# Optimization experiments

Hardware: AMD Instinct MI355X
Metric: run time of the kernel (lower is better)

The kernel has to match this reference:

```python
import jax, jax.numpy as jnp
import numpy as np

EPS_LN = 1e-5
EPS_BN = 1e-5

B, S, N, F, H, E, L = 8, 16, 1024, 16, 128, 32768, 4


def _layernorm(h, g, b):
    mu = h.mean(-1, keepdims=True)
    var = ((h - mu) ** 2).mean(-1, keepdims=True)
    return (h - mu) / jnp.sqrt(var + EPS_LN) * g + b


def setup_inputs() -> dict:
    key = jax.random.key(0)
    ks = iter(jax.random.split(key, 40))
    nrm = lambda shape, s=0.05: jax.random.normal(next(ks), shape, dtype=jnp.float32) * s
    inp = {
        'x': jax.random.normal(next(ks), (B, S, N, F), dtype=jnp.float32),
        'edge_index': jax.random.randint(next(ks), (2, E), 0, N, dtype=jnp.int32),
        'edge_weights': jax.random.uniform(next(ks), (E,), dtype=jnp.float32),
        'edge_features': jax.random.normal(next(ks), (E, 1), dtype=jnp.float32),
        # input projection: Linear(F,H) + LayerNorm(H)
        'w_in': nrm((F, H), 1.0 / np.sqrt(F)), 'b_in': nrm((H,)),
        'ln_in_g': jnp.ones((H,), jnp.float32), 'ln_in_b': jnp.zeros((H,), jnp.float32),
        # edge feature proj: Linear(1,H) -> ReLU -> Linear(H,1) -> Sigmoid
        'w_e1': nrm((1, H), 1.0), 'b_e1': nrm((H,)),
        'w_e2': nrm((H, 1), 1.0 / np.sqrt(H)), 'b_e2': nrm((1,)),
        # L GCN layers (weight [H,H], bias [H]) + BatchNorm1d affine params
        'gcn_w': nrm((L, H, H), 1.0 / np.sqrt(H)), 'gcn_b': nrm((L, H)),
        'bn_g': jnp.ones((L, H), jnp.float32), 'bn_b': jnp.zeros((L, H), jnp.float32),
        # 2-layer LSTM (PyTorch gate order i,f,g,o)
        'lstm_wih': nrm((2, 4 * H, H), 1.0 / np.sqrt(H)), 'lstm_whh': nrm((2, 4 * H, H), 1.0 / np.sqrt(H)),
        'lstm_bih': nrm((2, 4 * H)), 'lstm_bhh': nrm((2, 4 * H)),
        # output projection: Linear(H,H//2) + LayerNorm + Linear(H//2,1)
        'w_o1': nrm((H, H // 2), 1.0 / np.sqrt(H)), 'b_o1': nrm((H // 2,)),
        'ln_o_g': jnp.ones((H // 2,), jnp.float32), 'ln_o_b': jnp.zeros((H // 2,), jnp.float32),
        'w_o2': nrm((H // 2, 1), 1.0 / np.sqrt(H // 2)), 'b_o2': nrm((1,)),
    }
    return inp


def _forward(x, edge_index, edge_weights, edge_features,
             w_in, b_in, ln_in_g, ln_in_b, w_e1, b_e1, w_e2, b_e2,
             gcn_w, gcn_b, bn_g, bn_b,
             lstm_wih, lstm_whh, lstm_bih, lstm_bhh,
             w_o1, b_o1, ln_o_g, ln_o_b, w_o2, b_o2):
    Bs, Ss, Ns, Fs = x.shape
    BN = Bs * Ns
    # edge attention gating of edge weights
    e = jax.nn.relu(edge_features @ w_e1 + b_e1)
    att = jax.nn.sigmoid(e @ w_e2 + b_e2)[:, 0]            # [E]
    ew = edge_weights * att
    # input projection (dropout = identity in eval)
    h0 = jax.nn.relu(_layernorm(x @ w_in + b_in, ln_in_g, ln_in_b))   # [B,S,N,H]
    xf = h0.reshape(Bs * Ss, Ns, H)
    # replicate original slicing x[t:t+B] on the flattened (B*S) axis
    idx = jnp.arange(Ss)[:, None] + jnp.arange(Bs)[None, :]           # [S,B]
    hs = xf[idx].reshape(Ss, BN, H)                                   # [S,B*N,H]
    # GCN normalization (shared across timesteps): self-loops over all B*N nodes
    src = jnp.concatenate([edge_index[0], jnp.arange(BN, dtype=edge_index.dtype)])
    dst = jnp.concatenate([edge_index[1], jnp.arange(BN, dtype=edge_index.dtype)])
    w_sl = jnp.concatenate([ew, jnp.ones((BN,), ew.dtype)])
    deg = jax.ops.segment_sum(w_sl, dst, num_segments=BN)
    dis = jnp.where(deg > 0, jax.lax.rsqrt(jnp.where(deg > 0, deg, 1.0)), 0.0)
    norm = dis[src] * w_sl * dis[dst]                                  # [E+BN]
    # eval-mode BatchNorm (running mean 0, var 1)
    bn_scale = bn_g / np.sqrt(1.0 + EPS_BN)

    def gcn_block(h):                                                  # [BN,H]
        for l in range(L):
            identity = h
            hw = h @ gcn_w[l]
            m = jax.ops.segment_sum(hw[src] * norm[:, None], dst, num_segments=BN) + gcn_b[l]
            h = jax.nn.relu(m * bn_scale[l] + bn_b[l]) + identity
        return h

    hs = jax.vmap(gcn_block)(hs)                                       # [S,B*N,H]
    xt = jnp.transpose(hs.reshape(Ss, Bs, Ns, H), (1, 0, 2, 3))        # [B,S,N,H]
    # LSTM over the time axis for each (b,n) node sequence
    seq = jnp.transpose(xt, (0, 2, 1, 3)).reshape(BN, Ss, H)           # [B*N,S,H]

    def lstm_layer(seq, wih, whh, bih, bhh):
        def step(carry, xt):
            hprev, cprev = carry
            gates = xt @ wih.T + hprev @ whh.T + bih + bhh
            i, f, g, o = jnp.split(gates, 4, axis=-1)
            c = jax.nn.sigmoid(f) * cprev + jax.nn.sigmoid(i) * jnp.tanh(g)
            hn = jax.nn.sigmoid(o) * jnp.tanh(c)
            return (hn, c), hn
        z = jnp.zeros((seq.shape[0], H), seq.dtype)
        _, ys = jax.lax.scan(step, (z, z), jnp.swapaxes(seq, 0, 1))
        return jnp.swapaxes(ys, 0, 1)                                  # [B*N,S,H]

    y = lstm_layer(seq, lstm_wih[0], lstm_whh[0], lstm_bih[0], lstm_bhh[0])
    y = lstm_layer(y, lstm_wih[1], lstm_whh[1], lstm_bih[1], lstm_bhh[1])
    y = y[:, -1].reshape(Bs, Ns, H)
    z = jax.nn.relu(_layernorm(y @ w_o1 + b_o1, ln_o_g, ln_o_b))
    out = z @ w_o2 + b_o2                                              # [B,N,1]
    return out[..., None]                                              # [B,N,1,1]


def reference(x, edge_index, edge_weights, edge_features,
              w_in, b_in, ln_in_g, ln_in_b, w_e1, b_e1, w_e2, b_e2,
              gcn_w, gcn_b, bn_g, bn_b,
              lstm_wih, lstm_whh, lstm_bih, lstm_bhh,
              w_o1, b_o1, ln_o_g, ln_o_b, w_o2, b_o2):
    return _forward(x, edge_index, edge_weights, edge_features,
                    w_in, b_in, ln_in_g, ln_in_b, w_e1, b_e1, w_e2, b_e2,
                    gcn_w, gcn_b, bn_g, bn_b,
                    lstm_wih, lstm_whh, lstm_bih, lstm_bhh,
                    w_o1, b_o1, ln_o_g, ln_o_b, w_o2, b_o2)
```

## Files before the change

### kernel.cpp

```cpp
#include <hip/hip_runtime.h>
#include <cstdint>

#define EPS 1e-5f

typedef unsigned short ushort_t;
typedef __bf16 bf16x8 __attribute__((ext_vector_type(8)));
typedef float f32x4 __attribute__((ext_vector_type(4)));

__device__ __forceinline__ float sigm(float x) { return 1.f / (1.f + expf(-x)); }
__device__ __forceinline__ unsigned short f2bf(float f) {
    unsigned int u = __builtin_bit_cast(unsigned int, f);
    return (unsigned short)((u + 0x7fffu + ((u >> 16) & 1u)) >> 16);
}
__device__ __forceinline__ float bf2f(unsigned short s) {
    unsigned int u = ((unsigned int)s) << 16;
    return __builtin_bit_cast(float, u);
}
__device__ __forceinline__ float sigm_fast(float x) {
    float t = __builtin_amdgcn_exp2f(-1.44269504f * x);
    return __builtin_amdgcn_rcpf(1.f + t);
}
__device__ __forceinline__ float tanh_fast(float x) {
    float xc = fminf(fmaxf(x, -15.f), 15.f);
    float t = __builtin_amdgcn_exp2f(-2.88539008f * xc);
    return (1.f - t) * __builtin_amdgcn_rcpf(1.f + t);
}

__global__ __launch_bounds__(256) void edge_att_deg(const float* __restrict__ ef,
                                                    const float* __restrict__ we1,
                                                    const float* __restrict__ be1,
                                                    const float* __restrict__ we2,
                                                    const float* __restrict__ be2,
                                                    const float* __restrict__ ewin,
                                                    const int* __restrict__ dst,
                                                    float* __restrict__ ew,
                                                    float* __restrict__ deg) {
    int e = blockIdx.x * blockDim.x + threadIdx.x;
    if (e >= 32768) return;
    float x = ef[e];
    float acc = 0.f;
    for (int h = 0; h < 128; ++h) {
        float v = fmaxf(x * we1[h] + be1[h], 0.f);
        acc += v * we2[h];
    }
    float wv = ewin[e] * sigm(acc + be2[0]);
    ew[e] = wv;
    atomicAdd(&deg[dst[e]], wv);
}
__global__ __launch_bounds__(256) void make_dis(float* __restrict__ deg) {
    int i = blockIdx.x * blockDim.x + threadIdx.x;
    if (i < 1024) { float d = deg[i] + 1.0f; deg[i] = (d > 0.f) ? rsqrtf(d) : 0.f; }
}
__global__ __launch_bounds__(256) void scatterA(const int* __restrict__ src,
                                                const int* __restrict__ dst,
                                                const float* __restrict__ ew,
                                                const float* __restrict__ dis,
                                                float* __restrict__ A) {
    int e = blockIdx.x * blockDim.x + threadIdx.x;
    if (e >= 32768) return;
    int s = src[e], d = dst[e];
    atomicAdd(&A[d * 1024 + s], dis[s] * ew[e] * dis[d]);
}

__global__ __launch_bounds__(256) void convF2B(const float* __restrict__ s,
                                               ushort_t* __restrict__ d, int n) {
    int i = blockIdx.x * blockDim.x + threadIdx.x;
    if (i < n) d[i] = f2bf(s[i]);
}
__global__ __launch_bounds__(256) void conv_all(const float* __restrict__ gcnw,
                                                const float* __restrict__ wih,
                                                const float* __restrict__ whh,
                                                const float* __restrict__ bih,
                                                const float* __restrict__ bhh,
                                                ushort_t* __restrict__ gcnwT,
                                                ushort_t* __restrict__ wgi,
                                                ushort_t* __restrict__ wgh,
                                                float* __restrict__ bsg) {
    int i = blockIdx.x * 256 + threadIdx.x;
    if (i < 65536) {
        int l = i >> 14, rem = i & 16383, in = rem >> 7, outc = rem & 127;
        gcnwT[l * 16384 + outc * 128 + in] = f2bf(gcnw[i]);
        return;
    }
    int j = i - 65536;
    if (j < 131072) {
        int l = j >> 16, rem = j & 65535, c = rem >> 7, kx = rem & 127;
        int g = (c >> 4) & 3, h = (c >> 6) * 16 + (c & 15);
        int src = (l * 512 + g * 128 + h) * 128 + kx;
        wgi[j] = f2bf(wih[src]);
        wgh[j] = f2bf(whh[src]);
        return;
    }
    int b = j - 131072;
    if (b < 1024) {
        int l = b >> 9, c = b & 511;
        int g = (c >> 4) & 3, h = (c >> 6) * 16 + (c & 15);
        int src = l * 512 + g * 128 + h;
        bsg[b] = bih[src] + bhh[src];
    }
}

__global__ __launch_bounds__(256) void in_proj_ln(const float* __restrict__ x,
                                                  const float* __restrict__ w,
                                                  const float* __restrict__ bias,
                                                  const float* __restrict__ g,
                                                  const float* __restrict__ be,
                                                  ushort_t* __restrict__ hA,
                                                  ushort_t* __restrict__ hB) {
    int row = blockIdx.x * 4 + (threadIdx.x >> 6);
    int lane = threadIdx.x & 63;
    int k = row >> 10, n = row & 1023;
    float xv = x[(int64_t)row * 16 + (lane & 15)];
    float a0 = bias[lane], a1 = bias[lane + 64];
#pragma unroll
    for (int f = 0; f < 16; ++f) {
        float xf = __shfl(xv, f, 16);
        a0 += xf * w[f * 128 + lane];
        a1 += xf * w[f * 128 + lane + 64];
    }
    float s = a0 + a1;
#pragma unroll
    for (int off = 1; off < 64; off <<= 1) s += __shfl_xor(s, off, 64);
    float mu = s * (1.f / 128.f);
    float d0 = a0 - mu, d1 = a1 - mu;
    float vs = d0 * d0 + d1 * d1;
#pragma unroll
    for (int off = 1; off < 64; off <<= 1) vs += __shfl_xor(vs, off, 64);
    float rstd = rsqrtf(vs * (1.f / 128.f) + EPS);
    float v0 = fmaxf(d0 * rstd * g[lane] + be[lane], 0.f);
    float v1 = fmaxf(d1 * rstd * g[lane + 64] + be[lane + 64], 0.f);
    int64_t idx = ((int64_t)k * 1024 + n) * 128 + lane;
    ushort_t b0 = f2bf(v0), b1v = f2bf(v1);
    if (k < 16) { hA[idx] = b0; hA[idx + 64] = b1v; }
    hB[idx] = b0; hB[idx + 64] = b1v;
}

__global__ __launch_bounds__(256) void gemm_feat_t(const ushort_t* __restrict__ hA,
                                                   const ushort_t* __restrict__ Wt,
                                                   ushort_t* __restrict__ hwT) {
    __shared__ __align__(16) char AsB[32768];
    __shared__ __align__(16) char BsB[32768];
    const int tid = threadIdx.x, lane = tid & 63, wid = tid >> 6;
    const int wr = wid >> 1, wc = wid & 1, q = lane >> 4, l15 = lane & 15;
    const int t = blockIdx.y;
    const int row0 = blockIdx.x * 128;
    const ushort_t* Ap = hA + ((int64_t)t * 1024 + row0) * 128;
    f32x4 acc[4][4];
#pragma unroll
    for (int m = 0; m < 4; ++m)
#pragma unroll
        for (int n = 0; n < 4; ++n) acc[m][n] = f32x4{0.f, 0.f, 0.f, 0.f};
#pragma unroll
    for (int i = 0; i < 8; ++i) {
        int id = i * 256 + tid; int r = id >> 4, sg = id & 15;
        uint4 va = *(const uint4*)(Ap + r * 128 + sg * 8);
        *(uint4*)(AsB + r * 256 + ((sg * 16) ^ ((r & 7) << 4))) = va;
        uint4 vb = *(const uint4*)(Wt + r * 128 + sg * 8);
        *(uint4*)(BsB + r * 256 + ((sg * 16) ^ ((r & 7) << 4))) = vb;
    }
    __syncthreads();
#pragma unroll
    for (int kk = 0; kk < 4; ++kk) {
        bf16x8 af[4], bfr[4];
#pragma unroll
        for (int m = 0; m < 4; ++m) {
            int row = wr * 64 + m * 16 + l15;
            af[m] = __builtin_bit_cast(bf16x8,
                *(const uint4*)(AsB + row * 256 + ((kk * 64 + q * 16) ^ ((row & 7) << 4))));
        }
#pragma unroll
        for (int n = 0; n < 4; ++n) {
            int col = wc * 64 + n * 16 + l15;
            bfr[n] = __builtin_bit_cast(bf16x8,
                *(const uint4*)(BsB + col * 256 + ((kk * 64 + q * 16) ^ ((col & 7) << 4))));
        }
#pragma unroll
        for (int m = 0; m < 4; ++m)
#pragma unroll
            for (int n = 0; n < 4; ++n)
                acc[m][n] = __builtin_amdgcn_mfma_f32_16x16x32_bf16(af[m], bfr[n], acc[m][n], 0, 0, 0);
    }
#pragma unroll
    for (int m = 0; m < 4; ++m) {
        int bn = row0 + wr * 64 + m * 16 + q * 4;
#pragma unroll
        for (int n = 0; n < 4; ++n) {
            int col = wc * 64 + n * 16 + l15;
            ushort4 u;
            u.x = f2bf(acc[m][n][0]); u.y = f2bf(acc[m][n][1]);
            u.z = f2bf(acc[m][n][2]); u.w = f2bf(acc[m][n][3]);
            *(ushort4*)(hwT + ((int64_t)t * 128 + col) * 1024 + bn) = u;
        }
    }
}

__global__ __launch_bounds__(256) void gcn_layer(ushort_t* __restrict__ hA,
                                                 ushort_t* __restrict__ hB,
                                                 const ushort_t* __restrict__ Wt,
                                                 const ushort_t* __restrict__ Abf,
                                                 const ushort_t* __restrict__ hwT,
                                                 const float* __restrict__ dis,
                                                 const float* __restrict__ gcnb,
                                                 const float* __restrict__ bng,
                                                 const float* __restrict__ bnb) {
    __shared__ __align__(16) char AsB[16384];
    __shared__ __align__(16) char BsB[32768];
    const int tid = threadIdx.x, lane = tid & 63, wid = tid >> 6;
    const int wr = wid >> 1, wc = wid & 1, q = lane >> 4, l15 = lane & 15;
    const int bx = blockIdx.x;
    const bool adj = bx < 256;
    const int lb = adj ? bx : bx - 256;
    const int tt = lb >> 4;
    const int n0 = (lb & 15) * 64;
    ushort_t* Ap = (adj ? hA : hB) + ((int64_t)tt * 1024 + n0) * 128;

#pragma unroll
    for (int i = 0; i < 4; ++i) {
        int id = i * 256 + tid; int r = id >> 4, sg = id & 15;
        uint4 va = *(const uint4*)(Ap + r * 128 + sg * 8);
        *(uint4*)(AsB + r * 256 + ((sg * 16) ^ ((r & 7) << 4))) = va;
    }
#pragma unroll
    for (int i = 0; i < 8; ++i) {
        int id = i * 256 + tid; int r = id >> 4, sg = id & 15;
        uint4 vb = *(const uint4*)(Wt + r * 128 + sg * 8);
        *(uint4*)(BsB + r * 256 + ((sg * 16) ^ ((r & 7) << 4))) = vb;
    }
    __syncthreads();

    f32x4 accF[2][4];
#pragma unroll
    for (int m = 0; m < 2; ++m)
#pragma unroll
        for (int n = 0; n < 4; ++n) accF[m][n] = f32x4{0.f, 0.f, 0.f, 0.f};
#pragma unroll
    for (int kk = 0; kk < 4; ++kk) {
        bf16x8 af[2], bfr[4];
#pragma unroll
        for (int m = 0; m < 2; ++m) {
            int row = wr * 32 + m * 16 + l15;
            af[m] = __builtin_bit_cast(bf16x8,
                *(const uint4*)(AsB + row * 256 + ((kk * 64 + q * 16) ^ ((row & 7) << 4))));
        }
#pragma unroll
        for (int n = 0; n < 4; ++n) {
            int col = wc * 64 + n * 16 + l15;
            bfr[n] = __builtin_bit_cast(bf16x8,
                *(const uint4*)(BsB + col * 256 + ((kk * 64 + q * 16) ^ ((col & 7) << 4))));
        }
#pragma unroll
        for (int m = 0; m < 2; ++m)
#pragma unroll
            for (int n = 0; n < 4; ++n)
                accF[m][n] = __builtin_amdgcn_mfma_f32_16x16x32_bf16(af[m], bfr[n], accF[m][n], 0, 0, 0);
    }

    f32x4 accA[2][4];
#pragma unroll
    for (int m = 0; m < 2; ++m)
#pragma unroll
        for (int n = 0; n < 4; ++n) accA[m][n] = f32x4{0.f, 0.f, 0.f, 0.f};
    if (adj) {
        for (int k0 = 0; k0 < 1024; k0 += 64) {
            __syncthreads();
#pragma unroll
            for (int i = 0; i < 2; ++i) {
                int id = i * 256 + tid; int r = id >> 3, sg = id & 7;
                uint4 v = *(const uint4*)(Abf + (int64_t)(n0 + r) * 1024 + k0 + sg * 8);
                *(uint4*)(BsB + r * 128 + ((sg * 16) ^ ((r & 7) << 4))) = v;
            }
#pragma unroll
            for (int i = 0; i < 4; ++i) {
                int id = i * 256 + tid; int r = id >> 3, sg = id & 7;
                uint4 v = *(const uint4*)(hwT + (int64_t)tt * 131072 + (int64_t)r * 1024 + k0 + sg * 8);
                *(uint4*)(BsB + 8192 + r * 128 + ((sg * 16) ^ ((r & 7) << 4))) = v;
            }
            __syncthreads();
#pragma unroll
            for (int kk = 0; kk < 2; ++kk) {
                bf16x8 af2[2], bf2[4];
#pragma unroll
                for (int m = 0; m < 2; ++m) {
                    int row = wr * 32 + m * 16 + l15;
                    af2[m] = __builtin_bit_cast(bf16x8,
                        *(const uint4*)(BsB + row * 128 + ((kk * 64 + q * 16) ^ ((row & 7) << 4))));
                }
#pragma unroll
                for (int n = 0; n < 4; ++n) {
                    int col = wc * 64 + n * 16 + l15;
                    bf2[n] = __builtin_bit_cast(bf16x8,
                        *(const uint4*)(BsB + 8192 + col * 128 + ((kk * 64 + q * 16) ^ ((col & 7) << 4))));
                }
#pragma unroll
                for (int m = 0; m < 2; ++m)
#pragma unroll
                    for (int n = 0; n < 4; ++n)
                        accA[m][n] = __builtin_amdgcn_mfma_f32_16x16x32_bf16(af2[m], bf2[n], accA[m][n], 0, 0, 0);
            }
        }
    }
    __syncthreads();

    const float rs = rsqrtf(1.f + EPS);
#pragma unroll
    for (int n = 0; n < 4; ++n) {
        int col = wc * 64 + n * 16 + l15;
        float gb = gcnb[col], sc = bng[col] * rs, bb = bnb[col];
        int seg16 = (col >> 3) * 16, wb = (col & 7) * 2;
#pragma unroll
        for (int m = 0; m < 2; ++m) {
            int rl0 = wr * 32 + m * 16 + q * 4;
#pragma unroll
            for (int e = 0; e < 4; ++e) {
                int rl = rl0 + e;
                float sl = 1.f, ad = 0.f;
                if (adj) { float dv = dis[n0 + rl]; sl = dv * dv; ad = accA[m][n][e]; }
                float mv = sl * accF[m][n][e] + gb + ad;
                ushort_t rbv = *(const ushort_t*)(AsB + rl * 256 + (seg16 ^ ((rl & 7) << 4)) + wb);
                float v = fmaxf(mv * sc + bb, 0.f) + bf2f(rbv);
                *(ushort_t*)(BsB + rl * 256 + (seg16 ^ ((rl & 7) << 4)) + wb) = f2bf(v);
            }
        }
    }
    __syncthreads();
#pragma unroll
    for (int i = 0; i < 4; ++i) {
        int id = i * 256 + tid; int r = id >> 4, sg = id & 15;
        uint4 v = *(const uint4*)(BsB + r * 256 + ((sg * 16) ^ ((r & 7) << 4)));
        *(uint4*)(Ap + r * 128 + sg * 8) = v;
    }
}

template <int MODE>
__global__ __launch_bounds__(512, 2) void lstm_layer(
    const ushort_t* __restrict__ hA, const ushort_t* __restrict__ hB,
    const ushort_t* __restrict__ X,
    const ushort_t* __restrict__ Wi, const ushort_t* __restrict__ Wh,
    const float* __restrict__ bs,
    ushort_t* __restrict__ Y,
    const float* __restrict__ w1, const float* __restrict__ b1,
    const float* __restrict__ lg, const float* __restrict__ lb,
    const float* __restrict__ w2, const float* __restrict__ b2,
    float* __restrict__ out) {
    __shared__ __align__(16) char Xs[8192];
    __shared__ __align__(16) char Hs[8192];
    __shared__ __align__(16) char W1s[32768];
    const int tid = threadIdx.x, lane = tid & 63, w = tid >> 6;
    const int q = lane >> 4, l15 = lane & 15;
    const int row0 = blockIdx.x * 32;
    const int r = tid >> 4, sg = tid & 15;
    const int bb = row0 >> 10, n0 = row0 & 1023;

    *(uint4*)(Hs + tid * 16) = uint4{0, 0, 0, 0};
    if constexpr (MODE == 1) {
#pragma unroll
        for (int i = 0; i < 4; ++i)
            *(uint4*)(W1s + (i * 512 + tid) * 16) =
                *(const uint4*)((const char*)w1 + (i * 512 + tid) * 16);
    }
    bf16x8 wi[4][4], wh[4][4];
#pragma unroll
    for (int n = 0; n < 4; ++n)
#pragma unroll
        for (int kk = 0; kk < 4; ++kk) {
            int col = w * 64 + n * 16 + l15;
            wi[n][kk] = __builtin_bit_cast(bf16x8, *(const uint4*)(Wi + col * 128 + kk * 32 + q * 8));
            wh[n][kk] = __builtin_bit_cast(bf16x8, *(const uint4*)(Wh + col * 128 + kk * 32 + q * 8));
        }
    const int cb = w * 64 + l15;
    const float bi = bs[cb], bf = bs[cb + 16], bg = bs[cb + 32], bo = bs[cb + 48];
    const int k = w * 16 + l15;
    float c[2][4] = {};

    auto xsrc = [&](int t) -> const ushort_t* {
        if constexpr (MODE == 0)
            return (bb == 0) ? hA + ((int64_t)t * 1024 + n0) * 128
                             : hB + ((int64_t)(t + bb) * 1024 + n0) * 128;
        else
            return X + ((int64_t)t * 8192 + row0) * 128;
    };

    uint4 xn = *(const uint4*)(xsrc(0) + r * 128 + sg * 8);
    *(uint4*)(Xs + r * 256 + ((sg * 16) ^ ((r & 7) << 4))) = xn;
    __syncthreads();

    for (int t = 0; t < 16; ++t) {
        xn = *(const uint4*)(xsrc(t < 15 ? t + 1 : 15) + r * 128 + sg * 8);

        f32x4 acc[2][4];
#pragma unroll
        for (int m = 0; m < 2; ++m)
#pragma unroll
            for (int n = 0; n < 4; ++n) acc[m][n] = f32x4{0.f, 0.f, 0.f, 0.f};
#pragma unroll
        for (int kk = 0; kk < 4; ++kk) {
            bf16x8 ax[2], ah[2];
#pragma unroll
            for (int m = 0; m < 2; ++m) {
                int rw = m * 16 + l15;
                int off = rw * 256 + ((kk * 64 + q * 16) ^ ((rw & 7) << 4));
                ax[m] = __builtin_bit_cast(bf16x8, *(const uint4*)(Xs + off));
                ah[m] = __builtin_bit_cast(bf16x8, *(const uint4*)(Hs + off));
            }
#pragma unroll
            for (int n = 0; n < 4; ++n)
#pragma unroll
                for (int m = 0; m < 2; ++m) {
                    acc[m][n] = __builtin_amdgcn_mfma_f32_16x16x32_bf16(ax[m], wi[n][kk], acc[m][n], 0, 0, 0);
                    acc[m][n] = __builtin_amdgcn_mfma_f32_16x16x32_bf16(ah[m], wh[n][kk], acc[m][n], 0, 0, 0);
                }
        }
        __syncthreads();

        *(uint4*)(Xs + r * 256 + ((sg * 16) ^ ((r & 7) << 4))) = xn;
#pragma unroll
        for (int m = 0; m < 2; ++m)
#pragma unroll
            for (int e = 0; e < 4; ++e) {
                float ig = sigm_fast(acc[m][0][e] + bi);
                float fg = sigm_fast(acc[m][1][e] + bf);
                float gg = tanh_fast(acc[m][2][e] + bg);
                float og = sigm_fast(acc[m][3][e] + bo);
                float cn = fg * c[m][e] + ig * gg;
                c[m][e] = cn;
                float hn = og * tanh_fast(cn);
                int rw = m * 16 + q * 4 + e;
                int byte = rw * 256 + ((((k >> 3) * 16) ^ ((rw & 7) << 4)) | ((k & 7) * 2));
                *(ushort_t*)(Hs + byte) = f2bf(hn);
            }
        __syncthreads();

        if constexpr (MODE == 0) {
            uint4 v = *(const uint4*)(Hs + r * 256 + ((sg * 16) ^ ((r & 7) << 4)));
            *(uint4*)(Y + ((int64_t)t * 8192 + row0 + r) * 128 + sg * 8) = v;
        }
    }

    if constexpr (MODE == 1) {
        float accj[4] = {b1[sg * 4 + 0], b1[sg * 4 + 1], b1[sg * 4 + 2], b1[sg * 4 + 3]};
#pragma unroll
        for (int kb = 0; kb < 16; ++kb) {
            uint4 hv = *(const uint4*)(Hs + r * 256 + ((kb * 16) ^ ((r & 7) << 4)));
            const ushort_t* hp = (const ushort_t*)&hv;
#pragma unroll
            for (int j2 = 0; j2 < 8; ++j2) {
                float hval = bf2f(hp[j2]);
                int kx = kb * 8 + j2;
                f32x4 wv = *(const f32x4*)(W1s + kx * 256 + sg * 16);
                accj[0] += hval * wv[0]; accj[1] += hval * wv[1];
                accj[2] += hval * wv[2]; accj[3] += hval * wv[3];
            }
        }
        float s4 = accj[0] + accj[1] + accj[2] + accj[3];
        s4 += __shfl_xor(s4, 1); s4 += __shfl_xor(s4, 2);
        s4 += __shfl_xor(s4, 4); s4 += __shfl_xor(s4, 8);
        float mu = s4 * (1.f / 64.f);
        float d0 = accj[0] - mu, d1 = accj[1] - mu, d2 = accj[2] - mu, d3 = accj[3] - mu;
        float v4 = d0 * d0 + d1 * d1 + d2 * d2 + d3 * d3;
        v4 += __shfl_xor(v4, 1); v4 += __shfl_xor(v4, 2);
        v4 += __shfl_xor(v4, 4); v4 += __shfl_xor(v4, 8);
        float rstd = rsqrtf(v4 * (1.f / 64.f) + EPS);
        float dj[4] = {d0, d1, d2, d3};
        float p = 0.f;
#pragma unroll
        for (int j = 0; j < 4; ++j) {
            int jj = sg * 4 + j;
            float z = fmaxf(dj[j] * rstd * lg[jj] + lb[jj], 0.f);
            p += z * w2[jj];
        }
        p += __shfl_xor(p, 1); p += __shfl_xor(p, 2);
        p += __shfl_xor(p, 4); p += __shfl_xor(p, 8);
        if (sg == 0) out[row0 + r] = p + b2[0];
    }
}

extern "C" void kernel_launch(void* const* d_in, const int* in_sizes, int n_in,
                              void* d_out, int out_size, void* d_ws, size_t ws_size,
                              hipStream_t stream) {
    const float* x    = (const float*)d_in[0];
    const int*   eidx = (const int*)d_in[1];
    const float* ewt  = (const float*)d_in[2];
    const float* efeat= (const float*)d_in[3];
    const float* w_in = (const float*)d_in[4];
    const float* b_in = (const float*)d_in[5];
    const float* lng  = (const float*)d_in[6];
    const float* lnb  = (const float*)d_in[7];
    const float* we1  = (const float*)d_in[8];
    const float* be1  = (const float*)d_in[9];
    const float* we2  = (const float*)d_in[10];
    const float* be2  = (const float*)d_in[11];
    const float* gcnw = (const float*)d_in[12];
    const float* gcnb = (const float*)d_in[13];
    const float* bng  = (const float*)d_in[14];
    const float* bnb  = (const float*)d_in[15];
    const float* wih  = (const float*)d_in[16];
    const float* whh  = (const float*)d_in[17];
    const float* bih  = (const float*)d_in[18];
    const float* bhh  = (const float*)d_in[19];
    const float* wo1  = (const float*)d_in[20];
    const float* bo1  = (const float*)d_in[21];
    const float* lnog = (const float*)d_in[22];
    const float* lnob = (const float*)d_in[23];
    const float* wo2  = (const float*)d_in[24];
    const float* bo2  = (const float*)d_in[25];
    float* out = (float*)d_out;

    char* W = (char*)d_ws;
    ushort_t* hA        = (ushort_t*)(W);
    ushort_t* hB        = (ushort_t*)(W + (4ll << 20));
    ushort_t* y1        = (ushort_t*)(W + (10ll << 20));
    ushort_t* hwT       = (ushort_t*)(W + (42ll << 20));
    float*    Adense    = (float*)(W + (46ll << 20));
    ushort_t* Adense_bf = (ushort_t*)(W + (50ll << 20));
    float*    ew        = (float*)(W + (52ll << 20));
    float*    dis       = (float*)(W + (52ll << 20) + 0x20000);
    float*    bsg       = (float*)(W + (52ll << 20) + 0x21000);
    ushort_t* gcnwT     = (ushort_t*)(W + (52ll << 20) + 0x22000);
    ushort_t* wgi       = (ushort_t*)(W + (52ll << 20) + 0x42000);
    ushort_t* wgh       = (ushort_t*)(W + (52ll << 20) + 0x82000);

    const int* srcI = eidx;
    const int* dstI = eidx + 32768;

    hipMemsetAsync(dis, 0, 1024 * sizeof(float), stream);
    hipMemsetAsync(Adense, 0, 1048576 * sizeof(float), stream);
    edge_att_deg<<<128, 256, 0, stream>>>(efeat, we1, be1, we2, be2, ewt, dstI, ew, dis);
    make_dis<<<4, 256, 0, stream>>>(dis);
    scatterA<<<128, 256, 0, stream>>>(srcI, dstI, ew, dis, Adense);
    convF2B<<<4096, 256, 0, stream>>>(Adense, Adense_bf, 1048576);
    conv_all<<<772, 256, 0, stream>>>(gcnw, wih, whh, bih, bhh, gcnwT, wgi, wgh, bsg);

    in_proj_ln<<<5888, 256, 0, stream>>>(x, w_in, b_in, lng, lnb, hA, hB);

    for (int l = 0; l < 4; ++l) {
        gemm_feat_t<<<dim3(8, 16, 1), 256, 0, stream>>>(hA, gcnwT + l * 16384, hwT);
        gcn_layer<<<624, 256, 0, stream>>>(hA, hB, gcnwT + l * 16384, Adense_bf, hwT,
                                           dis, gcnb + l * 128, bng + l * 128, bnb + l * 128);
    }

    lstm_layer<0><<<256, 512, 0, stream>>>(hA, hB, nullptr, wgi, wgh, bsg, y1,
                                           nullptr, nullptr, nullptr, nullptr,
                                           nullptr, nullptr, nullptr);
    lstm_layer<1><<<256, 512, 0, stream>>>(nullptr, nullptr, y1,
                                           wgi + 65536, wgh + 65536, bsg + 512, nullptr,
                                           wo1, bo1, lnog, lnob, wo2, bo2, out);
}
```

Measured before the change: 250.0 us.

## Double-buffer LSTM X/H tiles and use direct global-to-LDS loads in GCN

The LSTM step kernel now ping-pongs its X and H shared-memory tiles. This drops the mid-step barrier: new h values and the prefetched next X go into the other buffer while the current one is still being read. The GCN adjacency loop replaces register-staged global-to-shared copies with global_load_lds 16-byte direct loads, keeping the XOR swizzle by permuting which segment each lane fetches. The cost is twice the LSTM shared memory, which may reduce occupancy headroom.

```diff
diff --git a/kernel.cpp b/kernel.cpp
--- a/kernel.cpp
+++ b/kernel.cpp
@@ -6,6 +6,10 @@
 typedef unsigned short ushort_t;
 typedef __bf16 bf16x8 __attribute__((ext_vector_type(8)));
 typedef float f32x4 __attribute__((ext_vector_type(4)));
+
+#define GLD16(gp, lp) __builtin_amdgcn_global_load_lds( \
+    (const __attribute__((address_space(1))) void*)(gp), \
+    (__attribute__((address_space(3))) void*)(lp), 16, 0, 0)
 
 __device__ __forceinline__ float sigm(float x) { return 1.f / (1.f + expf(-x)); }
 __device__ __forceinline__ unsigned short f2bf(float f) {
@@ -261,19 +265,21 @@
 #pragma unroll
         for (int n = 0; n < 4; ++n) accA[m][n] = f32x4{0.f, 0.f, 0.f, 0.f};
     if (adj) {
+        const int rl8 = lane >> 3;
+        const int sgg = (lane & 7) ^ rl8;
         for (int k0 = 0; k0 < 1024; k0 += 64) {
             __syncthreads();
 #pragma unroll
             for (int i = 0; i < 2; ++i) {
-                int id = i * 256 + tid; int r = id >> 3, sg = id & 7;
-                uint4 v = *(const uint4*)(Abf + (int64_t)(n0 + r) * 1024 + k0 + sg * 8);
-                *(uint4*)(BsB + r * 128 + ((sg * 16) ^ ((r & 7) << 4))) = v;
+                int r = i * 32 + wid * 8 + rl8;
+                GLD16(Abf + (int64_t)(n0 + r) * 1024 + k0 + sgg * 8,
+                      BsB + (i * 32 + wid * 8) * 128);
             }
 #pragma unroll
             for (int i = 0; i < 4; ++i) {
-                int id = i * 256 + tid; int r = id >> 3, sg = id & 7;
-                uint4 v = *(const uint4*)(hwT + (int64_t)tt * 131072 + (int64_t)r * 1024 + k0 + sg * 8);
-                *(uint4*)(BsB + 8192 + r * 128 + ((sg * 16) ^ ((r & 7) << 4))) = v;
+                int r = i * 32 + wid * 8 + rl8;
+                GLD16(hwT + (int64_t)tt * 131072 + (int64_t)r * 1024 + k0 + sgg * 8,
+                      BsB + 8192 + (i * 32 + wid * 8) * 128);
             }
             __syncthreads();
 #pragma unroll
@@ -342,8 +348,8 @@
     const float* __restrict__ lg, const float* __restrict__ lb,
     const float* __restrict__ w2, const float* __restrict__ b2,
     float* __restrict__ out) {
-    __shared__ __align__(16) char Xs[8192];
-    __shared__ __align__(16) char Hs[8192];
+    __shared__ __align__(16) char Xs[16384];
+    __shared__ __align__(16) char Hs[16384];
     __shared__ __align__(16) char W1s[32768];
     const int tid = threadIdx.x, lane = tid & 63, w = tid >> 6;
     const int q = lane >> 4, l15 = lane & 15;
@@ -380,12 +386,16 @@
             return X + ((int64_t)t * 8192 + row0) * 128;
     };
 
-    uint4 xn = *(const uint4*)(xsrc(0) + r * 128 + sg * 8);
-    *(uint4*)(Xs + r * 256 + ((sg * 16) ^ ((r & 7) << 4))) = xn;
+    {
+        uint4 x0 = *(const uint4*)(xsrc(0) + r * 128 + sg * 8);
+        *(uint4*)(Xs + r * 256 + ((sg * 16) ^ ((r & 7) << 4))) = x0;
+    }
     __syncthreads();
 
     for (int t = 0; t < 16; ++t) {
-        xn = *(const uint4*)(xsrc(t < 15 ? t + 1 : 15) + r * 128 + sg * 8);
+        const int p = (t & 1) * 8192, pn = ((t + 1) & 1) * 8192;
+        uint4 xn;
+        if (t < 15) xn = *(const uint4*)(xsrc(t + 1) + r * 128 + sg * 8);
 
         f32x4 acc[2][4];
 #pragma unroll
@@ -399,8 +409,8 @@
             for (int m = 0; m < 2; ++m) {
                 int rw = m * 16 + l15;
                 int off = rw * 256 + ((kk * 64 + q * 16) ^ ((rw & 7) << 4));
-                ax[m] = __builtin_bit_cast(bf16x8, *(const uint4*)(Xs + off));
-                ah[m] = __builtin_bit_cast(bf16x8, *(const uint4*)(Hs + off));
+                ax[m] = __builtin_bit_cast(bf16x8, *(const uint4*)(Xs + p + off));
+                ah[m] = __builtin_bit_cast(bf16x8, *(const uint4*)(Hs + p + off));
             }
 #pragma unroll
             for (int n = 0; n < 4; ++n)
@@ -410,9 +420,6 @@
                     acc[m][n] = __builtin_amdgcn_mfma_f32_16x16x32_bf16(ah[m], wh[n][kk], acc[m][n], 0, 0, 0);
                 }
         }
-        __syncthreads();
-
-        *(uint4*)(Xs + r * 256 + ((sg * 16) ^ ((r & 7) << 4))) = xn;
 #pragma unroll
         for (int m = 0; m < 2; ++m)
 #pragma unroll
@@ -426,12 +433,14 @@
                 float hn = og * tanh_fast(cn);
                 int rw = m * 16 + q * 4 + e;
                 int byte = rw * 256 + ((((k >> 3) * 16) ^ ((rw & 7) << 4)) | ((k & 7) * 2));
-                *(ushort_t*)(Hs + byte) = f2bf(hn);
-            }
+                *(ushort_t*)(Hs + pn + byte) = f2bf(hn);
+            }
+        if (t < 15)
+            *(uint4*)(Xs + pn + r * 256 + ((sg * 16) ^ ((r & 7) << 4))) = xn;
         __syncthreads();
 
         if constexpr (MODE == 0) {
-            uint4 v = *(const uint4*)(Hs + r * 256 + ((sg * 16) ^ ((r & 7) << 4)));
+            uint4 v = *(const uint4*)(Hs + pn + r * 256 + ((sg * 16) ^ ((r & 7) << 4)));
             *(uint4*)(Y + ((int64_t)t * 8192 + row0 + r) * 128 + sg * 8) = v;
         }
     }
@@ -461,16 +470,16 @@
         v4 += __shfl_xor(v4, 4); v4 += __shfl_xor(v4, 8);
         float rstd = rsqrtf(v4 * (1.f / 64.f) + EPS);
         float dj[4] = {d0, d1, d2, d3};
-        float p = 0.f;
+        float p2 = 0.f;
 #pragma unroll
         for (int j = 0; j < 4; ++j) {
             int jj = sg * 4 + j;
             float z = fmaxf(dj[j] * rstd * lg[jj] + lb[jj], 0.f);
-            p += z * w2[jj];
-        }
-        p += __shfl_xor(p, 1); p += __shfl_xor(p, 2);
-        p += __shfl_xor(p, 4); p += __shfl_xor(p, 8);
-        if (sg == 0) out[row0 + r] = p + b2[0];
+            p2 += z * w2[jj];
+        }
+        p2 += __shfl_xor(p2, 1); p2 += __shfl_xor(p2, 2);
+        p2 += __shfl_xor(p2, 4); p2 += __shfl_xor(p2, 8);
+        if (sg == 0) out[row0 + r] = p2 + b2[0];
     }
 }
 
```

Result: no change. 247.7 us, median of 2 (-0.9%).
